# Kernel tuning notes

Measured on AMD Instinct MI355X. Metric: run time of the kernel, lower is better.

The kernel has to match this reference:

```python
import jax, jax.numpy as jnp
import numpy as np
import math

SCALES = (0.25, 0.125, 0.0625, 0.03125)
CANONICAL_SIZE = 20.0
OUT_SIZE = (5, 5, 5)
SAMPLING_RATIO = 2


def _trilinear(f, pts):
    # f: [C, D0, D1, D2]; pts: [P, 3] in feature-map coords. Returns [C, P].
    Df = jnp.asarray(f.shape[1:], pts.dtype)
    Di = jnp.asarray(f.shape[1:], jnp.int32)
    # ROIAlign convention: samples with any coord < -1 or > D contribute 0.
    valid = jnp.all((pts > -1.0) & (pts < Df), axis=-1)  # [P]
    p = jnp.clip(pts, 0.0, Df - 1.0)
    p0 = jnp.floor(p)
    fr = p - p0                                  # [P,3]
    i0 = p0.astype(jnp.int32)
    i1 = jnp.minimum(i0 + 1, Di - 1)
    w = jnp.stack([1.0 - fr, fr], 0)             # [2,P,3]
    ii = jnp.stack([i0, i1], 0)                  # [2,P,3]
    acc = jnp.zeros((f.shape[0], pts.shape[0]), f.dtype)
    for a in (0, 1):
        for b in (0, 1):
            for c in (0, 1):
                wgt = w[a, :, 0] * w[b, :, 1] * w[c, :, 2]        # [P]
                val = f[:, ii[a, :, 0], ii[b, :, 1], ii[c, :, 2]]  # [C,P]
                acc = acc + val * wgt[None, :]
    return acc * valid[None, :].astype(f.dtype)


def _axis_samples(n, sr):
    # normalized sub-sample centers in (0,1), flattened bin-major: [n*sr]
    bins = jnp.arange(n, dtype=jnp.float32)
    sub = (jnp.arange(sr, dtype=jnp.float32) + 0.5) / sr
    return ((bins[:, None] + sub[None, :]) / n).reshape(-1)


def _pool_one(feats, bidx, roi7, scale):
    # feats: [B,C,D0,D1,D2]; roi7 = [c0,c1,c2,s0,s1,s2,angle_deg]
    f = feats[bidx]                              # [C,D0,D1,D2]
    ctr = roi7[0:3] * scale
    size = roi7[3:6] * scale
    theta = roi7[6] * (math.pi / 180.0)          # pooler op converts deg -> rad
    os0, os1, os2 = OUT_SIZE
    sr = SAMPLING_RATIO
    g0 = (_axis_samples(os0, sr) - 0.5) * size[0]
    g1 = (_axis_samples(os1, sr) - 0.5) * size[1]
    g2 = (_axis_samples(os2, sr) - 0.5) * size[2]
    O0, O1, O2 = jnp.meshgrid(g0, g1, g2, indexing='ij')
    c, s = jnp.cos(theta), jnp.sin(theta)
    # rotation in the (axis0, axis1) plane of the permuted roi coords
    r0 = c * O0 - s * O1
    r1 = s * O0 + c * O1
    pts = jnp.stack([ctr[0] + r0, ctr[1] + r1, ctr[2] + O2], -1)  # [os0*sr,os1*sr,os2*sr,3]
    sampled = _trilinear(f, pts.reshape(-1, 3))                    # [C, P]
    C = f.shape[0]
    sampled = sampled.reshape(C, os0, sr, os1, sr, os2, sr)
    return sampled.mean(axis=(2, 4, 6))          # [C, os0, os1, os2]


def setup_inputs() -> dict:
    key = jax.random.key(0)
    k = jax.random.split(key, 10)
    B, C, R = 2, 64, 128
    x0 = jax.random.normal(k[0], (B, C, 64, 64, 64), jnp.float32)
    x1 = jax.random.normal(k[1], (B, C, 32, 32, 32), jnp.float32)
    x2 = jax.random.normal(k[2], (B, C, 16, 16, 16), jnp.float32)
    x3 = jax.random.normal(k[3], (B, C, 8, 8, 8), jnp.float32)
    ctr = jax.random.uniform(k[4], (R, 3), jnp.float32, 20.0, 236.0)
    dxy = jax.random.uniform(k[5], (R, 2), jnp.float32, 1.0, 16.0)
    dz = jax.random.uniform(k[6], (R, 1), jnp.float32, 1.0, 8.0)
    theta = jax.random.uniform(k[7], (R, 1), jnp.float32, -math.pi, math.pi)
    bbox3d = jnp.concatenate([ctr, dxy, dz, theta], axis=1)  # standard: [x,y,z,dx,dy,dz,theta]
    batch_ids = jax.random.randint(k[8], (R,), 0, B, jnp.int32)
    return {"x0": x0, "x1": x1, "x2": x2, "x3": x3, "bbox3d": bbox3d, "batch_ids": batch_ids}


def reference(x0, x1, x2, x3, bbox3d, batch_ids):
    b = bbox3d
    # convert_to_roi_format: permute [0,2,1,3,5,4,6,7] (drop id col here), angle rad->deg
    roi7 = jnp.stack([b[:, 1], b[:, 0], b[:, 2], b[:, 4], b[:, 3], b[:, 5],
                      b[:, 6] * (180.0 / math.pi)], axis=1)
    # LevelMapper_3d
    size = jnp.sqrt(jnp.maximum(b[:, 3], b[:, 4]))
    rate = size / CANONICAL_SIZE
    levels = jnp.argmin(jnp.abs(jnp.asarray(SCALES, jnp.float32)[None, :] - rate[:, None]), axis=1)
    feats = [x0, x1, x2, x3]
    R, C = roi7.shape[0], x0.shape[1]
    os0, os1, os2 = OUT_SIZE
    result = jnp.zeros((R, C, os0, os1, os2), x0.dtype)
    for l in range(len(SCALES)):
        pooled = jax.vmap(lambda r, bi: _pool_one(feats[l], bi, r, SCALES[l]))(roi7, batch_ids)
        mask = (levels == l)[:, None, None, None, None]
        result = jnp.where(mask, pooled, result)
    return result
```

## Files before the change

### kernel.cpp

```cpp
#include <hip/hip_runtime.h>
#include <math.h>

#define CHB 8
#define C_NUM 64
#define NCELL 125
#define MAX_VOX 256
#define NITEMS 250

__device__ __forceinline__ int swz(int L) { return L ^ ((L >> 3) & 7); }

__device__ __forceinline__ void acc8(const float4* __restrict__ rg4, int v, float w,
                                     float4& A, float4& B) {
    int P = swz(v * 2);
    float4 lo = rg4[P];
    float4 hi = rg4[P ^ 1];
    A.x = fmaf(lo.x, w, A.x); A.y = fmaf(lo.y, w, A.y);
    A.z = fmaf(lo.z, w, A.z); A.w = fmaf(lo.w, w, A.w);
    B.x = fmaf(hi.x, w, B.x); B.y = fmaf(hi.y, w, B.y);
    B.z = fmaf(hi.z, w, B.z); B.w = fmaf(hi.w, w, B.w);
}

__global__ __launch_bounds__(256) void pooler_kernel(
    const float* __restrict__ x0, const float* __restrict__ x1,
    const float* __restrict__ x2, const float* __restrict__ x3,
    const float* __restrict__ bbox, const int* __restrict__ bids,
    float* __restrict__ out)
{
    __shared__ float reg[MAX_VOX * CHB];
    __shared__ float partial[NITEMS * 9];

    const int blk = blockIdx.x;
    const int r   = blk >> 3;
    const int cg  = blk & 7;
    const int tid = threadIdx.x;

    const float b0 = bbox[r*7+0], b1 = bbox[r*7+1], b2 = bbox[r*7+2];
    const float b3 = bbox[r*7+3], b4 = bbox[r*7+4], b5 = bbox[r*7+5];
    const float b6 = bbox[r*7+6];
    const int bid  = bids[r];

    const float rate = sqrtf(fmaxf(b3, b4)) / 20.0f;
    const float SC[4] = {0.25f, 0.125f, 0.0625f, 0.03125f};
    int lvl = 0;
    float best = fabsf(SC[0] - rate);
    #pragma unroll
    for (int j = 1; j < 4; ++j) {
        float d = fabsf(SC[j] - rate);
        if (d < best) { best = d; lvl = j; }
    }
    const float scale = SC[lvl];

    const float* f; int D;
    if (lvl == 0)      { f = x0; D = 64; }
    else if (lvl == 1) { f = x1; D = 32; }
    else if (lvl == 2) { f = x2; D = 16; }
    else               { f = x3; D = 8;  }
    const float Df = (float)D;

    const float ctr0 = b1 * scale;
    const float ctr1 = b0 * scale;
    const float ctr2 = b2 * scale;
    const float sz0  = b4 * scale;
    const float sz1  = b3 * scale;
    const float sz2  = b5 * scale;
    const float theta = (b6 * (180.0f / (float)M_PI)) * ((float)M_PI / 180.0f);
    float st, ct;
    sincosf(theta, &st, &ct);

    const float hx = 0.451f * (fabsf(ct) * sz0 + fabsf(st) * sz1) + 0.01f;
    const float hy = 0.451f * (fabsf(st) * sz0 + fabsf(ct) * sz1) + 0.01f;
    const float hz = 0.451f * sz2 + 0.01f;
    const int x_lo = (int)fminf(fmaxf(ctr0 - hx, 0.0f), Df - 1.0f);
    const int y_lo = (int)fminf(fmaxf(ctr1 - hy, 0.0f), Df - 1.0f);
    const int z_lo = (int)fminf(fmaxf(ctr2 - hz, 0.0f), Df - 1.0f);
    const int x_hi = (int)fminf(fmaxf(ctr0 + hx, 0.0f), Df - 1.0f);
    const int y_hi = (int)fminf(fmaxf(ctr1 + hy, 0.0f), Df - 1.0f);
    const int z_hi = (int)fminf(fmaxf(ctr2 + hz, 0.0f), Df - 1.0f);

    const int nx = min(x_hi - x_lo + 2, D - x_lo);
    const int ny = min(y_hi - y_lo + 2, D - y_lo);
    const int nz = min(z_hi - z_lo + 2, D - z_lo);

    int RX2 = 2; while (RX2 < nx) RX2 <<= 1; RX2 = min(RX2, 8);
    int RY2 = 2; while (RY2 < ny) RY2 <<= 1; RY2 = min(RY2, 8);
    int RZ2 = 2; while (RZ2 < nz) RZ2 <<= 1; RZ2 = min(RZ2, 4);
    const int lz  = __builtin_ctz(RZ2);
    const int ly  = __builtin_ctz(RY2);
    const int lx  = __builtin_ctz(RX2);
    const int sxs = lz + ly;
    const int lnv = lx + ly + lz;
    const int nvox = 1 << lnv;

    const size_t vox = (size_t)D * D * D;
    const float* fbase = f + ((size_t)bid * C_NUM + (size_t)cg * CHB) * vox;
    const int total_e = nvox * CHB;
    for (int e = tid; e < total_e; e += 256) {
        int ch = e >> lnv;
        int v  = e & (nvox - 1);
        int rz = v & (RZ2 - 1);
        int ry = (v >> lz) & (RY2 - 1);
        int rx = v >> sxs;
        int gx = min(x_lo + rx, D - 1);
        int gy = min(y_lo + ry, D - 1);
        int gz = min(z_lo + rz, D - 1);
        float val = fbase[(size_t)ch * vox + (size_t)(gx * D + gy) * D + gz];
        int P = swz(v * 2 + (ch >> 2));
        reg[P * 4 + (ch & 3)] = val;
    }
    __syncthreads();

    if (tid < NITEMS) {
        const int cell  = tid >> 1;
        const int shalf = tid & 1;
        const int i0 = cell / 25;
        const int rem = cell - i0 * 25;
        const int i1 = rem / 5;
        const int i2 = rem - i1 * 5;

        float4 accA = make_float4(0.f, 0.f, 0.f, 0.f);
        float4 accB = make_float4(0.f, 0.f, 0.f, 0.f);
        const float4* rg4 = (const float4*)reg;

        #pragma unroll
        for (int s = 0; s < 4; ++s) {
            const int s0 = shalf, s1 = (s >> 1) & 1, s2 = s & 1;
            float u0 = ((float)i0 + ((float)s0 + 0.5f) * 0.5f) / 5.0f;
            float u1 = ((float)i1 + ((float)s1 + 0.5f) * 0.5f) / 5.0f;
            float u2 = ((float)i2 + ((float)s2 + 0.5f) * 0.5f) / 5.0f;
            float g0 = (u0 - 0.5f) * sz0;
            float g1 = (u1 - 0.5f) * sz1;
            float g2 = (u2 - 0.5f) * sz2;
            float px = ctr0 + (ct * g0 - st * g1);
            float py = ctr1 + (st * g0 + ct * g1);
            float pz = ctr2 + g2;
            float validf = ((px > -1.0f) && (px < Df) &&
                            (py > -1.0f) && (py < Df) &&
                            (pz > -1.0f) && (pz < Df)) ? 1.0f : 0.0f;
            float q0 = fminf(fmaxf(px, 0.0f), Df - 1.0f);
            float q1 = fminf(fmaxf(py, 0.0f), Df - 1.0f);
            float q2 = fminf(fmaxf(pz, 0.0f), Df - 1.0f);
            int A0 = (int)q0, A1 = (int)q1, A2 = (int)q2;
            float f0 = q0 - (float)A0;
            float f1 = q1 - (float)A1;
            float f2 = q2 - (float)A2;
            int d0 = ((A0 + 1 < D) ? 1 : 0) << sxs;
            int d1 = ((A1 + 1 < D) ? 1 : 0) << lz;
            int d2 = (A2 + 1 < D) ? 1 : 0;
            int base = ((A0 - x_lo) << sxs) + ((A1 - y_lo) << lz) + (A2 - z_lo);

            float wx0 = 1.0f - f0, wx1 = f0;
            float wy0 = 1.0f - f1, wy1 = f1;
            float wz0 = (1.0f - f2) * validf, wz1 = f2 * validf;
            float w00 = wx0 * wy0, w01 = wx0 * wy1;
            float w10 = wx1 * wy0, w11 = wx1 * wy1;

            acc8(rg4, base,                w00 * wz0, accA, accB);
            acc8(rg4, base + d2,           w00 * wz1, accA, accB);
            acc8(rg4, base + d1,           w01 * wz0, accA, accB);
            acc8(rg4, base + d1 + d2,      w01 * wz1, accA, accB);
            acc8(rg4, base + d0,           w10 * wz0, accA, accB);
            acc8(rg4, base + d0 + d2,      w10 * wz1, accA, accB);
            acc8(rg4, base + d0 + d1,      w11 * wz0, accA, accB);
            acc8(rg4, base + d0 + d1 + d2, w11 * wz1, accA, accB);
        }

        const int pb = tid * 9;
        partial[pb + 0] = accA.x; partial[pb + 1] = accA.y;
        partial[pb + 2] = accA.z; partial[pb + 3] = accA.w;
        partial[pb + 4] = accB.x; partial[pb + 5] = accB.y;
        partial[pb + 6] = accB.z; partial[pb + 7] = accB.w;
    }
    __syncthreads();

    float4* ob4 = (float4*)(out + (size_t)r * (C_NUM * NCELL) + (size_t)cg * (CHB * NCELL));
    for (int q = tid; q < 250; q += 256) {
        float vres[4];
        #pragma unroll
        for (int j = 0; j < 4; ++j) {
            int o = q * 4 + j;
            unsigned ch = (unsigned)o / 125u;
            int cell = o - (int)ch * 125;
            vres[j] = (partial[(cell * 2) * 9 + ch] +
                       partial[(cell * 2 + 1) * 9 + ch]) * 0.125f;
        }
        ob4[q] = make_float4(vres[0], vres[1], vres[2], vres[3]);
    }
}

extern "C" void kernel_launch(void* const* d_in, const int* in_sizes, int n_in,
                              void* d_out, int out_size, void* d_ws, size_t ws_size,
                              hipStream_t stream) {
    const float* x0   = (const float*)d_in[0];
    const float* x1   = (const float*)d_in[1];
    const float* x2   = (const float*)d_in[2];
    const float* x3   = (const float*)d_in[3];
    const float* bbox = (const float*)d_in[4];
    const int*   bids = (const int*)d_in[5];
    float* out = (float*)d_out;

    hipLaunchKernelGGL(pooler_kernel, dim3(1024), dim3(256), 0, stream,
                       x0, x1, x2, x3, bbox, bids, out);
}
```

Baseline: 190.2 us.

## Factor trilinear sampling into separable xy-bilinear columns then z-lerp

Exploits that the rotation only affects the xy plane. The kernel now precomputes xy bilinear offsets and weights for the 100 sample columns and z offsets and weights for the 10 z samples. It then builds interpolated per-column, per-z-row channel values in shared memory, and finishes each output with a short z lerp. This replaces the 8-corner gather per sample with a 4-corner bilinear stage shared across z plus a 2-tap stage, at the cost of extra shared memory and another block barrier.

Measured after the change: 184.8 us. 1.03x faster.

```diff
diff --git a/kernel.cpp b/kernel.cpp
--- a/kernel.cpp
+++ b/kernel.cpp
@@ -6,18 +6,37 @@
 #define NCELL 125
 #define MAX_VOX 256
 #define NITEMS 250
+#define NXY 100
+#define NZS 10
+#define CSTR 202
 
 __device__ __forceinline__ int swz(int L) { return L ^ ((L >> 3) & 7); }
 
-__device__ __forceinline__ void acc8(const float4* __restrict__ rg4, int v, float w,
-                                     float4& A, float4& B) {
-    int P = swz(v * 2);
-    float4 lo = rg4[P];
-    float4 hi = rg4[P ^ 1];
-    A.x = fmaf(lo.x, w, A.x); A.y = fmaf(lo.y, w, A.y);
-    A.z = fmaf(lo.z, w, A.z); A.w = fmaf(lo.w, w, A.w);
-    B.x = fmaf(hi.x, w, B.x); B.y = fmaf(hi.y, w, B.y);
-    B.z = fmaf(hi.z, w, B.z); B.w = fmaf(hi.w, w, B.w);
+__device__ __forceinline__ float4 bil4(const float4 w, const float4 a, const float4 b,
+                                       const float4 c, const float4 d) {
+    float4 r;
+    r.x = fmaf(w.x, a.x, fmaf(w.y, b.x, fmaf(w.z, c.x, w.w * d.x)));
+    r.y = fmaf(w.x, a.y, fmaf(w.y, b.y, fmaf(w.z, c.y, w.w * d.y)));
+    r.z = fmaf(w.x, a.z, fmaf(w.y, b.z, fmaf(w.z, c.z, w.w * d.z)));
+    r.w = fmaf(w.x, a.w, fmaf(w.y, b.w, fmaf(w.z, c.w, w.w * d.w)));
+    return r;
+}
+
+__device__ __forceinline__ void lerpacc(const float4* __restrict__ cg4,
+                                        const int2 zoo, const float2 zww, const int s,
+                                        float4& A, float4& B) {
+    const float4 a0 = cg4[zoo.x + s];
+    const float4 a1 = cg4[zoo.y + s];
+    const float4 b0 = cg4[zoo.x + (s ^ 1)];
+    const float4 b1 = cg4[zoo.y + (s ^ 1)];
+    A.x = fmaf(zww.x, a0.x, fmaf(zww.y, a1.x, A.x));
+    A.y = fmaf(zww.x, a0.y, fmaf(zww.y, a1.y, A.y));
+    A.z = fmaf(zww.x, a0.z, fmaf(zww.y, a1.z, A.z));
+    A.w = fmaf(zww.x, a0.w, fmaf(zww.y, a1.w, A.w));
+    B.x = fmaf(zww.x, b0.x, fmaf(zww.y, b1.x, B.x));
+    B.y = fmaf(zww.x, b0.y, fmaf(zww.y, b1.y, B.y));
+    B.z = fmaf(zww.x, b0.z, fmaf(zww.y, b1.z, B.z));
+    B.w = fmaf(zww.x, b0.w, fmaf(zww.y, b1.w, B.w));
 }
 
 __global__ __launch_bounds__(256) void pooler_kernel(
@@ -26,8 +45,13 @@
     const float* __restrict__ bbox, const int* __restrict__ bids,
     float* __restrict__ out)
 {
-    __shared__ float reg[MAX_VOX * CHB];
-    __shared__ float partial[NITEMS * 9];
+    __shared__ float  reg[MAX_VOX * CHB];
+    __shared__ float4 col4[3 * CSTR + 200];
+    __shared__ float  partial[NITEMS * 9];
+    __shared__ int4   gvb[NXY];
+    __shared__ float4 gw4[NXY];
+    __shared__ int2   gzo[NZS];
+    __shared__ float2 gzw[NZS];
 
     const int blk = blockIdx.x;
     const int r   = blk >> 3;
@@ -90,6 +114,43 @@
     const int sxs = lz + ly;
     const int lnv = lx + ly + lz;
     const int nvox = 1 << lnv;
+
+    if (tid < NXY) {
+        const int t0 = tid / 10;
+        const int t1 = tid - t0 * 10;
+        const float u0 = ((float)t0 + 0.5f) * 0.1f;
+        const float u1 = ((float)t1 + 0.5f) * 0.1f;
+        const float g0 = (u0 - 0.5f) * sz0;
+        const float g1 = (u1 - 0.5f) * sz1;
+        const float px = ctr0 + (ct * g0 - st * g1);
+        const float py = ctr1 + (st * g0 + ct * g1);
+        const float vxy = ((px > -1.0f) && (px < Df) &&
+                           (py > -1.0f) && (py < Df)) ? 1.0f : 0.0f;
+        const float q0 = fminf(fmaxf(px, 0.0f), Df - 1.0f);
+        const float q1 = fminf(fmaxf(py, 0.0f), Df - 1.0f);
+        const int A0 = (int)q0, A1 = (int)q1;
+        const float f0 = q0 - (float)A0;
+        const float f1 = q1 - (float)A1;
+        const int d0 = ((A0 + 1 < D) ? 1 : 0) << sxs;
+        const int d1 = ((A1 + 1 < D) ? 1 : 0) << lz;
+        const int vb = ((A0 - x_lo) << sxs) + ((A1 - y_lo) << lz);
+        gvb[tid] = make_int4(vb * 2, (vb + d1) * 2, (vb + d0) * 2, (vb + d0 + d1) * 2);
+        const float wx0 = 1.0f - f0, wy0 = 1.0f - f1;
+        gw4[tid] = make_float4(wx0 * wy0 * vxy, wx0 * f1 * vxy,
+                               f0  * wy0 * vxy, f0  * f1 * vxy);
+    } else if (tid < NXY + NZS) {
+        const int t2 = tid - NXY;
+        const float u2 = ((float)t2 + 0.5f) * 0.1f;
+        const float pz = ctr2 + (u2 - 0.5f) * sz2;
+        const float vz = ((pz > -1.0f) && (pz < Df)) ? 1.0f : 0.0f;
+        const float q2 = fminf(fmaxf(pz, 0.0f), Df - 1.0f);
+        const int A2 = (int)q2;
+        const float f2 = q2 - (float)A2;
+        const int dz = (A2 + 1 < D) ? 1 : 0;
+        const int zr0 = A2 - z_lo;
+        gzo[t2] = make_int2(zr0 * CSTR, (zr0 + dz) * CSTR);
+        gzw[t2] = make_float2((1.0f - f2) * vz, f2 * vz);
+    }
 
     const size_t vox = (size_t)D * D * D;
     const float* fbase = f + ((size_t)bid * C_NUM + (size_t)cg * CHB) * vox;
@@ -109,60 +170,49 @@
     }
     __syncthreads();
 
+    const float4* rg4 = (const float4*)reg;
+
+    const int nit = NXY << lz;
+    for (int it = tid; it < nit; it += 256) {
+        const int zr  = (int)(((unsigned)it * 656u) >> 16);
+        const int t01 = it - zr * 100;
+        const int4   vb = gvb[t01];
+        const float4 w  = gw4[t01];
+        const int zz = zr * 2;
+        const int p00 = swz(vb.x + zz);
+        const int p01 = swz(vb.y + zz);
+        const int p10 = swz(vb.z + zz);
+        const int p11 = swz(vb.w + zz);
+        const float4 lo = bil4(w, rg4[p00], rg4[p01], rg4[p10], rg4[p11]);
+        const float4 hi = bil4(w, rg4[p00 ^ 1], rg4[p01 ^ 1], rg4[p10 ^ 1], rg4[p11 ^ 1]);
+        const int cw = swz(t01 * 2);
+        col4[zr * CSTR + cw]       = lo;
+        col4[zr * CSTR + (cw ^ 1)] = hi;
+    }
+    __syncthreads();
+
     if (tid < NITEMS) {
-        const int cell  = tid >> 1;
-        const int shalf = tid & 1;
+        const int cell = tid >> 1;
+        const int sh   = tid & 1;
         const int i0 = cell / 25;
         const int rem = cell - i0 * 25;
         const int i1 = rem / 5;
         const int i2 = rem - i1 * 5;
 
+        const int ta = (i0 * 2 + sh) * 10 + i1 * 2;
+        const int sA = swz(ta * 2);
+        const int sB = swz((ta + 1) * 2);
+        const int2   zoA = gzo[i2 * 2];
+        const int2   zoB = gzo[i2 * 2 + 1];
+        const float2 zwA = gzw[i2 * 2];
+        const float2 zwB = gzw[i2 * 2 + 1];
+
         float4 accA = make_float4(0.f, 0.f, 0.f, 0.f);
         float4 accB = make_float4(0.f, 0.f, 0.f, 0.f);
-        const float4* rg4 = (const float4*)reg;
-
-        #pragma unroll
-        for (int s = 0; s < 4; ++s) {
-            const int s0 = shalf, s1 = (s >> 1) & 1, s2 = s & 1;
-            float u0 = ((float)i0 + ((float)s0 + 0.5f) * 0.5f) / 5.0f;
-            float u1 = ((float)i1 + ((float)s1 + 0.5f) * 0.5f) / 5.0f;
-            float u2 = ((float)i2 + ((float)s2 + 0.5f) * 0.5f) / 5.0f;
-            float g0 = (u0 - 0.5f) * sz0;
-            float g1 = (u1 - 0.5f) * sz1;
-            float g2 = (u2 - 0.5f) * sz2;
-            float px = ctr0 + (ct * g0 - st * g1);
-            float py = ctr1 + (st * g0 + ct * g1);
-            float pz = ctr2 + g2;
-            float validf = ((px > -1.0f) && (px < Df) &&
-                            (py > -1.0f) && (py < Df) &&
-                            (pz > -1.0f) && (pz < Df)) ? 1.0f : 0.0f;
-            float q0 = fminf(fmaxf(px, 0.0f), Df - 1.0f);
-            float q1 = fminf(fmaxf(py, 0.0f), Df - 1.0f);
-            float q2 = fminf(fmaxf(pz, 0.0f), Df - 1.0f);
-            int A0 = (int)q0, A1 = (int)q1, A2 = (int)q2;
-            float f0 = q0 - (float)A0;
-            float f1 = q1 - (float)A1;
-            float f2 = q2 - (float)A2;
-            int d0 = ((A0 + 1 < D) ? 1 : 0) << sxs;
-            int d1 = ((A1 + 1 < D) ? 1 : 0) << lz;
-            int d2 = (A2 + 1 < D) ? 1 : 0;
-            int base = ((A0 - x_lo) << sxs) + ((A1 - y_lo) << lz) + (A2 - z_lo);
-
-            float wx0 = 1.0f - f0, wx1 = f0;
-            float wy0 = 1.0f - f1, wy1 = f1;
-            float wz0 = (1.0f - f2) * validf, wz1 = f2 * validf;
-            float w00 = wx0 * wy0, w01 = wx0 * wy1;
-            float w10 = wx1 * wy0, w11 = wx1 * wy1;
-
-            acc8(rg4, base,                w00 * wz0, accA, accB);
-            acc8(rg4, base + d2,           w00 * wz1, accA, accB);
-            acc8(rg4, base + d1,           w01 * wz0, accA, accB);
-            acc8(rg4, base + d1 + d2,      w01 * wz1, accA, accB);
-            acc8(rg4, base + d0,           w10 * wz0, accA, accB);
-            acc8(rg4, base + d0 + d2,      w10 * wz1, accA, accB);
-            acc8(rg4, base + d0 + d1,      w11 * wz0, accA, accB);
-            acc8(rg4, base + d0 + d1 + d2, w11 * wz1, accA, accB);
-        }
+        lerpacc(col4, zoA, zwA, sA, accA, accB);
+        lerpacc(col4, zoB, zwB, sA, accA, accB);
+        lerpacc(col4, zoA, zwA, sB, accA, accB);
+        lerpacc(col4, zoB, zwB, sB, accA, accB);
 
         const int pb = tid * 9;
         partial[pb + 0] = accA.x; partial[pb + 1] = accA.y;
```
